# Kernel tuning notes

Measured on AMD Instinct MI355X. Metric: run time of the kernel, lower is better.

The kernel has to match this reference:

```python
import jax, jax.numpy as jnp
import numpy as np

NEG_SLOPE = 0.2  # PyG GATConv default leaky_relu slope
EPS = 1e-16


def gat_conv(x, W, att_src, att_dst, bias, src, dst, num_nodes, heads, out_ch, concat):
    # x: [N, F_in]; W: [F_in, heads*out_ch]
    h = (x @ W).reshape(num_nodes, heads, out_ch)          # [N, H, C]
    a_src = jnp.sum(h * att_src, axis=-1)                  # [N, H]
    a_dst = jnp.sum(h * att_dst, axis=-1)                  # [N, H]
    alpha = jax.nn.leaky_relu(a_src[src] + a_dst[dst], NEG_SLOPE)  # [E, H]
    # segment softmax over incoming edges of each destination node
    amax = jax.ops.segment_max(alpha, dst, num_segments=num_nodes)  # [N, H]
    ex = jnp.exp(alpha - amax[dst])                        # [E, H]
    denom = jax.ops.segment_sum(ex, dst, num_segments=num_nodes)    # [N, H]
    attn = ex / (denom[dst] + EPS)                         # [E, H]
    msg = h[src] * attn[:, :, None]                        # [E, H, C]
    out = jax.ops.segment_sum(msg, dst, num_segments=num_nodes)     # [N, H, C]
    if concat:
        out = out.reshape(num_nodes, heads * out_ch)
    else:
        out = out.mean(axis=1)
    return out + bias


def setup_inputs() -> dict:
    key = jax.random.key(0)
    ks = jax.random.split(key, 10)
    N, E, F_in, H, C, OUT = 50000, 800000, 512, 4, 64, 40
    x = jax.random.normal(ks[0], (N, F_in), dtype=jnp.float32)
    edge_index = jax.random.randint(ks[1], (2, E), 0, N, dtype=jnp.int64)
    s1 = (2.0 / (F_in + H * C)) ** 0.5
    s2 = (2.0 / (H * C + OUT)) ** 0.5
    return {
        "x": x,
        "edge_index": edge_index,
        "W1": jax.random.normal(ks[2], (F_in, H * C), dtype=jnp.float32) * s1,
        "att_src1": jax.random.normal(ks[3], (H, C), dtype=jnp.float32) * 0.1,
        "att_dst1": jax.random.normal(ks[4], (H, C), dtype=jnp.float32) * 0.1,
        "b1": jnp.zeros((H * C,), dtype=jnp.float32),
        "W2": jax.random.normal(ks[5], (H * C, OUT), dtype=jnp.float32) * s2,
        "att_src2": jax.random.normal(ks[6], (1, OUT), dtype=jnp.float32) * 0.1,
        "att_dst2": jax.random.normal(ks[7], (1, OUT), dtype=jnp.float32) * 0.1,
        "b2": jnp.zeros((OUT,), dtype=jnp.float32),
    }


def reference(x, edge_index, W1, att_src1, att_dst1, b1, W2, att_src2, att_dst2, b2):
    N = x.shape[0]
    H, C = att_src1.shape
    OUT = att_src2.shape[1]
    # PyG GATConv default: add self-loops
    loops = jnp.arange(N, dtype=edge_index.dtype)
    src = jnp.concatenate([edge_index[0], loops])
    dst = jnp.concatenate([edge_index[1], loops])
    # dropout is identity in eval mode
    h = gat_conv(x, W1, att_src1, att_dst1, b1, src, dst, N, H, C, concat=True)
    h = jax.nn.elu(h)
    out = gat_conv(h, W2, att_src2, att_dst2, b2, src, dst, N, 1, OUT, concat=False)
    return jax.nn.log_softmax(out, axis=1)
```

## Files before the change

kernel.cpp:

```cpp
#include <hip/hip_runtime.h>
#include <math.h>

#define FIN   512
#define H1DIM 256
#define HEADS 4
#define CH    64
#define OUTC  40
#define NEG   0.2f
#define EPSV  1e-16f
#define BK    64

__device__ __forceinline__ float leaky(float a) { return fmaxf(a, NEG * a); }

__device__ __forceinline__ short f2bf(float f) {
    unsigned u = __builtin_bit_cast(unsigned, f);
    u += 0x7FFFu + ((u >> 16) & 1u);
    return (short)(u >> 16);
}
__device__ __forceinline__ float bf2f(short s) {
    return __builtin_bit_cast(float, ((unsigned)(unsigned short)s) << 16);
}
__device__ __forceinline__ unsigned cvtpk(float lo, float hi) {
    unsigned r;
    asm("v_cvt_pk_bf16_f32 %0, %1, %2" : "=v"(r) : "v"(lo), "v"(hi));
    return r;
}
__device__ __forceinline__ float lo16(unsigned u) {
    return __builtin_bit_cast(float, u << 16);
}
__device__ __forceinline__ float hi16(unsigned u) {
    return __builtin_bit_cast(float, u & 0xffff0000u);
}

typedef __attribute__((ext_vector_type(2))) float floatx2;

__device__ __forceinline__ unsigned f32x2_to_fp8x2(float a, float b) {
    return (unsigned)__builtin_amdgcn_cvt_pk_fp8_f32(a, b, 0, false);
}
template <bool HI>
__device__ __forceinline__ floatx2 fp8x2_to_f32(unsigned u) {
    return __builtin_amdgcn_cvt_pk_f32_fp8((int)u, HI);
}

typedef __attribute__((ext_vector_type(8))) short short8;
typedef __attribute__((ext_vector_type(4))) short short4_t;
typedef __attribute__((ext_vector_type(4))) float float4_t;

typedef unsigned int u32;
typedef const __attribute__((address_space(1))) u32 gu32;
typedef __attribute__((address_space(3))) u32 lu32;

__device__ __forceinline__ void load_lds16(const void* g, void* l) {
    __builtin_amdgcn_global_load_lds((gu32*)g, (lu32*)l, 16, 0, 0);
}

__global__ void cvt_w1_kernel(const float* __restrict__ W1, short* __restrict__ w1t)
{
    int idx = blockIdx.x * 256 + threadIdx.x;
    if (idx >= FIN * H1DIM) return;
    int k = idx >> 8;
    int n = idx & 255;
    w1t[(size_t)n * FIN + k] = f2bf(W1[idx]);
}

__global__ __launch_bounds__(256, 1) void gemm1_mfma_kernel(
    const float* __restrict__ x, const short* __restrict__ w1t,
    const float* __restrict__ attS, const float* __restrict__ attD,
    unsigned char* __restrict__ h1f, float* __restrict__ aS1, float* __restrict__ aD1, int N)
{
    __shared__ float As[64 * 512];

    const int tid  = threadIdx.x;
    const int lane = tid & 63;
    const int wid  = tid >> 6;
    const int row0 = blockIdx.x * 64;
    const int col0 = wid * 64;
    const int quad = lane >> 4;
    const int m16  = lane & 15;

#pragma unroll
    for (int inst = 0; inst < 32; ++inst) {
        int c   = inst * 256 + tid;
        int row = c >> 7;
        int q   = (c & 127) ^ (row & 7);
        int gr  = row0 + row; if (gr >= N) gr = N - 1;
        load_lds16(x + (size_t)gr * FIN + q * 4, (char*)As + c * 16);
    }
    __syncthreads();

    const short* bp[4];
#pragma unroll
    for (int j = 0; j < 4; ++j)
        bp[j] = w1t + (size_t)(col0 + j * 16 + m16) * FIN + quad * 8;

    float4_t acc[4][4];
#pragma unroll
    for (int i = 0; i < 4; ++i)
#pragma unroll
        for (int j = 0; j < 4; ++j) acc[i][j] = (float4_t){0.f, 0.f, 0.f, 0.f};

    short8 bcur[2][4];
#pragma unroll
    for (int half = 0; half < 2; ++half)
#pragma unroll
        for (int j = 0; j < 4; ++j)
            bcur[half][j] = *(const short8*)(bp[j] + half * 32);

#pragma unroll
    for (int kk = 0; kk < FIN / BK; ++kk) {
        short8 bnext[2][4];
        if (kk < FIN / BK - 1) {
#pragma unroll
            for (int half = 0; half < 2; ++half)
#pragma unroll
                for (int j = 0; j < 4; ++j)
                    bnext[half][j] = *(const short8*)(bp[j] + (kk + 1) * BK + half * 32);
        }
#pragma unroll
        for (int half = 0; half < 2; ++half) {
            short8 a[4];
#pragma unroll
            for (int i = 0; i < 4; ++i) {
                int row = i * 16 + m16;
                int cb  = kk * 16 + (quad + 4 * half) * 2;
                const char* rp = (const char*)As + row * 2048;
                float4 f0 = *(const float4*)(rp + ((cb ^ (row & 7)) * 16));
                float4 f1 = *(const float4*)(rp + (((cb + 1) ^ (row & 7)) * 16));
                unsigned* tp = (unsigned*)&a[i];
                tp[0] = cvtpk(f0.x, f0.y);
                tp[1] = cvtpk(f0.z, f0.w);
                tp[2] = cvtpk(f1.x, f1.y);
                tp[3] = cvtpk(f1.z, f1.w);
            }
#pragma unroll
            for (int i = 0; i < 4; ++i)
#pragma unroll
                for (int j = 0; j < 4; ++j)
                    acc[i][j] = __builtin_amdgcn_mfma_f32_16x16x32_bf16(a[i], bcur[half][j], acc[i][j], 0, 0, 0);
        }
        if (kk < FIN / BK - 1) {
#pragma unroll
            for (int half = 0; half < 2; ++half)
#pragma unroll
                for (int j = 0; j < 4; ++j)
                    bcur[half][j] = bnext[half][j];
        }
    }

    float attSv[4], attDv[4];
#pragma unroll
    for (int j = 0; j < 4; ++j) {
        attSv[j] = attS[col0 + j * 16 + m16];
        attDv[j] = attD[col0 + j * 16 + m16];
    }

    __syncthreads();
    unsigned char* Asb = (unsigned char*)As;

#pragma unroll
    for (int i = 0; i < 4; ++i) {
#pragma unroll
        for (int r = 0; r < 4; ++r) {
            int rloc = i * 16 + quad * 4 + r;
            unsigned pa = f32x2_to_fp8x2(acc[i][0][r], acc[i][1][r]);
            unsigned pb = f32x2_to_fp8x2(acc[i][2][r], acc[i][3][r]);
            int cb = rloc * 256 + col0 + m16;
            Asb[cb]      = (unsigned char)(pa & 0xff);
            Asb[cb + 16] = (unsigned char)((pa >> 8) & 0xff);
            Asb[cb + 32] = (unsigned char)(pb & 0xff);
            Asb[cb + 48] = (unsigned char)((pb >> 8) & 0xff);

            float ps = acc[i][0][r] * attSv[0] + acc[i][1][r] * attSv[1]
                     + acc[i][2][r] * attSv[2] + acc[i][3][r] * attSv[3];
            float pd = acc[i][0][r] * attDv[0] + acc[i][1][r] * attDv[1]
                     + acc[i][2][r] * attDv[2] + acc[i][3][r] * attDv[3];
#pragma unroll
            for (int off = 1; off < 16; off <<= 1) {
                ps += __shfl_xor(ps, off);
                pd += __shfl_xor(pd, off);
            }
            int row = row0 + rloc;
            if (m16 == 0 && row < N) {
                aS1[(size_t)row * 4 + wid] = ps;
                aD1[(size_t)row * 4 + wid] = pd;
            }
        }
    }
    __syncthreads();

#pragma unroll
    for (int inst = 0; inst < 4; ++inst) {
        int flat = inst * 4096 + tid * 16;
        int row  = flat >> 8;
        if (row0 + row < N)
            *(float4*)(h1f + (size_t)row0 * H1DIM + flat) = *(const float4*)(Asb + flat);
    }
}

__global__ void degcount_kernel(const int* __restrict__ ei, int* __restrict__ deg,
                                int* __restrict__ rank, int E, int Etot)
{
    int e = blockIdx.x * 256 + threadIdx.x;
    if (e >= Etot) return;
    int d = (e < E) ? ei[E + e] : (e - E);
    rank[e] = atomicAdd(&deg[d], 1);
}

__global__ __launch_bounds__(1024) void scan_partial_kernel(
    const int* __restrict__ deg, int* __restrict__ offsets,
    int* __restrict__ bsums, int N)
{
    __shared__ int wsums[16];
    __shared__ int excl[16];
    int tid = threadIdx.x, lane = tid & 63, wid = tid >> 6;
    int idx = blockIdx.x * 1024 + tid;
    int v = (idx < N) ? deg[idx] : 0;
    int sv = v;
#pragma unroll
    for (int off = 1; off < 64; off <<= 1) {
        int t = __shfl_up(sv, off, 64);
        if (lane >= off) sv += t;
    }
    if (lane == 63) wsums[wid] = sv;
    __syncthreads();
    if (wid == 0 && lane < 16) {
        int wv = wsums[lane];
        int sw = wv;
#pragma unroll
        for (int off = 1; off < 16; off <<= 1) {
            int t = __shfl_up(sw, off, 64);
            if (lane >= off) sw += t;
        }
        excl[lane] = sw - wv;
        if (lane == 15) bsums[blockIdx.x] = sw;
    }
    __syncthreads();
    if (idx < N) offsets[idx + 1] = sv + excl[wid];
}

__global__ __launch_bounds__(1024) void scan_tops_kernel(
    int* __restrict__ bsums, int* __restrict__ boffs, int nb)
{
    __shared__ int wsums[16];
    __shared__ int excl[16];
    int tid = threadIdx.x, lane = tid & 63, wid = tid >> 6;
    int v = (tid < nb) ? bsums[tid] : 0;
    int sv = v;
#pragma unroll
    for (int off = 1; off < 64; off <<= 1) {
        int t = __shfl_up(sv, off, 64);
        if (lane >= off) sv += t;
    }
    if (lane == 63) wsums[wid] = sv;
    __syncthreads();
    if (wid == 0 && lane < 16) {
        int wv = wsums[lane];
        int sw = wv;
#pragma unroll
        for (int off = 1; off < 16; off <<= 1) {
            int t = __shfl_up(sw, off, 64);
            if (lane >= off) sw += t;
        }
        excl[lane] = sw - wv;
    }
    __syncthreads();
    if (tid < nb) boffs[tid] = sv + excl[wid] - v;
}

__global__ __launch_bounds__(1024) void scan_add_kernel(
    int* __restrict__ offsets, const int* __restrict__ boffs, int N)
{
    int idx = blockIdx.x * 1024 + threadIdx.x;
    if (idx == 0) offsets[0] = 0;
    if (idx < N) offsets[idx + 1] += boffs[blockIdx.x];
}

__global__ void scatter_kernel(const int* __restrict__ ei, const int* __restrict__ offsets,
                               const int* __restrict__ rank, int* __restrict__ csr_src,
                               int E, int Etot)
{
    int e = blockIdx.x * 256 + threadIdx.x;
    if (e >= Etot) return;
    int s, d;
    if (e < E) { s = ei[e]; d = ei[E + e]; }
    else       { s = e - E; d = s; }
    csr_src[offsets[d] + rank[e]] = s;
}

__global__ __launch_bounds__(256) void agg1_kernel(
    const unsigned char* __restrict__ h1f, const float* __restrict__ aS,
    const float* __restrict__ aD, const int* __restrict__ offsets,
    const int* __restrict__ csr_src, const float* __restrict__ b1,
    short* __restrict__ g1b, int N)
{
    int lane = threadIdx.x & 63, wid = threadIdx.x >> 6;
    int half = lane >> 5;
    int l32  = lane & 31;
    int n = blockIdx.x * 4 + wid;
    if (n >= N) return;
    int start = offsets[n], end = offsets[n + 1];
    int h = l32 >> 3;
    int cbase = l32 * 8;
    float adh = aD[(size_t)n * 4 + h];

    float ac[8];
#pragma unroll
    for (int c = 0; c < 8; ++c) ac[c] = 0.f;
    float denom = 0.f;

    int p = start;
    for (; p + 4 <= end; p += 4) {
        int sA0 = csr_src[p],     sB0 = csr_src[p + 1];
        int sA1 = csr_src[p + 2], sB1 = csr_src[p + 3];
        int s0 = half ? sB0 : sA0;
        int s1 = half ? sB1 : sA1;
        float t0 = aS[(size_t)s0 * 4 + h] + adh;
        float t1 = aS[(size_t)s1 * 4 + h] + adh;
        uint2 r0 = *(const uint2*)&h1f[(size_t)s0 * H1DIM + cbase];
        uint2 r1 = *(const uint2*)&h1f[(size_t)s1 * H1DIM + cbase];
        float w0 = __expf(leaky(t0));
        float w1 = __expf(leaky(t1));
        denom += w0 + w1;
        floatx2 d0a = fp8x2_to_f32<false>(r0.x), d0b = fp8x2_to_f32<true>(r0.x);
        floatx2 d0c = fp8x2_to_f32<false>(r0.y), d0d = fp8x2_to_f32<true>(r0.y);
        floatx2 d1a = fp8x2_to_f32<false>(r1.x), d1b = fp8x2_to_f32<true>(r1.x);
        floatx2 d1c = fp8x2_to_f32<false>(r1.y), d1d = fp8x2_to_f32<true>(r1.y);
        ac[0] += w0 * d0a.x + w1 * d1a.x;
        ac[1] += w0 * d0a.y + w1 * d1a.y;
        ac[2] += w0 * d0b.x + w1 * d1b.x;
        ac[3] += w0 * d0b.y + w1 * d1b.y;
        ac[4] += w0 * d0c.x + w1 * d1c.x;
        ac[5] += w0 * d0c.y + w1 * d1c.y;
        ac[6] += w0 * d0d.x + w1 * d1d.x;
        ac[7] += w0 * d0d.y + w1 * d1d.y;
    }
    for (; p + 2 <= end; p += 2) {
        int sA = csr_src[p], sB = csr_src[p + 1];
        int s = half ? sB : sA;
        float t = aS[(size_t)s * 4 + h] + adh;
        uint2 r = *(const uint2*)&h1f[(size_t)s * H1DIM + cbase];
        float w = __expf(leaky(t));
        denom += w;
        floatx2 da = fp8x2_to_f32<false>(r.x), db = fp8x2_to_f32<true>(r.x);
        floatx2 dc = fp8x2_to_f32<false>(r.y), dd = fp8x2_to_f32<true>(r.y);
        ac[0] += w * da.x; ac[1] += w * da.y;
        ac[2] += w * db.x; ac[3] += w * db.y;
        ac[4] += w * dc.x; ac[5] += w * dc.y;
        ac[6] += w * dd.x; ac[7] += w * dd.y;
    }
    if (p < end) {
        int s = csr_src[p];
        float t = aS[(size_t)s * 4 + h] + adh;
        uint2 r = *(const uint2*)&h1f[(size_t)s * H1DIM + cbase];
        float w = half ? 0.f : __expf(leaky(t));
        denom += w;
        floatx2 da = fp8x2_to_f32<false>(r.x), db = fp8x2_to_f32<true>(r.x);
        floatx2 dc = fp8x2_to_f32<false>(r.y), dd = fp8x2_to_f32<true>(r.y);
        ac[0] += w * da.x; ac[1] += w * da.y;
        ac[2] += w * db.x; ac[3] += w * db.y;
        ac[4] += w * dc.x; ac[5] += w * dc.y;
        ac[6] += w * dd.x; ac[7] += w * dd.y;
    }

    denom += __shfl_xor(denom, 32);
#pragma unroll
    for (int c = 0; c < 8; ++c) ac[c] += __shfl_xor(ac[c], 32);

    if (half == 0) {
        float inv = 1.f / (denom + EPSV);
        float4 b0 = *(const float4*)&b1[cbase];
        float4 b4 = *(const float4*)&b1[cbase + 4];
        float v[8];
        v[0] = ac[0] * inv + b0.x;
        v[1] = ac[1] * inv + b0.y;
        v[2] = ac[2] * inv + b0.z;
        v[3] = ac[3] * inv + b0.w;
        v[4] = ac[4] * inv + b4.x;
        v[5] = ac[5] * inv + b4.y;
        v[6] = ac[6] * inv + b4.z;
        v[7] = ac[7] * inv + b4.w;
#pragma unroll
        for (int c = 0; c < 8; ++c) v[c] = v[c] > 0.f ? v[c] : expm1f(v[c]);
        short8 o;
        unsigned* op = (unsigned*)&o;
        op[0] = cvtpk(v[0], v[1]);
        op[1] = cvtpk(v[2], v[3]);
        op[2] = cvtpk(v[4], v[5]);
        op[3] = cvtpk(v[6], v[7]);
        *(short8*)&g1b[(size_t)n * H1DIM + cbase] = o;
    }
}

__global__ __launch_bounds__(256) void gemm2_kernel(
    const short* __restrict__ g1b, const float* __restrict__ W2,
    const float* __restrict__ attS2, const float* __restrict__ attD2,
    short* __restrict__ h2b, float* __restrict__ aS2, float* __restrict__ aD2, int N)
{
    __shared__ float rows[4][8][256];
    int lane = threadIdx.x & 63, wid = threadIdx.x >> 6;
    int nbase = blockIdx.x * 32 + wid * 8;
    bool act = lane < OUTC;
    int cc = act ? lane : 0;
    float attS = act ? attS2[lane] : 0.f;
    float attD = act ? attD2[lane] : 0.f;

#pragma unroll
    for (int i = 0; i < 8; ++i) {
        int n = nbase + i;
        float4 v = make_float4(0.f, 0.f, 0.f, 0.f);
        if (n < N) {
            short4_t hv = *(const short4_t*)&g1b[(size_t)n * H1DIM + lane * 4];
            v = make_float4(bf2f(hv[0]), bf2f(hv[1]), bf2f(hv[2]), bf2f(hv[3]));
        }
        *(float4*)&rows[wid][i][lane * 4] = v;
    }

    float acc[8];
#pragma unroll
    for (int i = 0; i < 8; ++i) acc[i] = 0.f;

    for (int k = 0; k < H1DIM; k += 4) {
        float w0 = W2[(size_t)(k + 0) * OUTC + cc];
        float w1 = W2[(size_t)(k + 1) * OUTC + cc];
        float w2 = W2[(size_t)(k + 2) * OUTC + cc];
        float w3 = W2[(size_t)(k + 3) * OUTC + cc];
#pragma unroll
        for (int i = 0; i < 8; ++i) {
            float4 g = *(const float4*)&rows[wid][i][k];
            acc[i] += g.x * w0 + g.y * w1 + g.z * w2 + g.w * w3;
        }
    }

#pragma unroll
    for (int i = 0; i < 8; ++i) {
        int n = nbase + i;
        if (n >= N) continue;
        if (act) h2b[(size_t)n * OUTC + lane] = f2bf(acc[i]);
        float ts = act ? acc[i] * attS : 0.f;
        float td = act ? acc[i] * attD : 0.f;
#pragma unroll
        for (int off = 32; off > 0; off >>= 1) {
            ts += __shfl_xor(ts, off);
            td += __shfl_xor(td, off);
        }
        if (lane == 0) { aS2[n] = ts; aD2[n] = td; }
    }
}

__global__ __launch_bounds__(256) void agg2_kernel(
    const short* __restrict__ h2b, const float* __restrict__ aS2,
    const float* __restrict__ aD2, const int* __restrict__ offsets,
    const int* __restrict__ csr_src, const float* __restrict__ b2,
    float* __restrict__ out, int N)
{
    int lane = threadIdx.x & 63, wid = threadIdx.x >> 6;
    int n = blockIdx.x * 4 + wid;
    if (n >= N) return;
    int start = offsets[n], end = offsets[n + 1];
    bool act = lane < OUTC;
    int cc = act ? lane : 0;
    float ad = aD2[n];

    float acc = 0.f, denom = 0.f;
    int p = start;
    for (; p + 4 <= end; p += 4) {
        int s0 = csr_src[p], s1 = csr_src[p + 1], s2 = csr_src[p + 2], s3 = csr_src[p + 3];
        float w0 = __expf(leaky(aS2[s0] + ad));
        float w1 = __expf(leaky(aS2[s1] + ad));
        float w2 = __expf(leaky(aS2[s2] + ad));
        float w3 = __expf(leaky(aS2[s3] + ad));
        short v0 = h2b[(size_t)s0 * OUTC + cc];
        short v1 = h2b[(size_t)s1 * OUTC + cc];
        short v2 = h2b[(size_t)s2 * OUTC + cc];
        short v3 = h2b[(size_t)s3 * OUTC + cc];
        denom += w0 + w1 + w2 + w3;
        acc += w0 * bf2f(v0) + w1 * bf2f(v1) + w2 * bf2f(v2) + w3 * bf2f(v3);
    }
    for (; p < end; ++p) {
        int s = csr_src[p];
        float w = __expf(leaky(aS2[s] + ad));
        denom += w;
        acc += w * bf2f(h2b[(size_t)s * OUTC + cc]);
    }

    float v = acc / (denom + EPSV) + (act ? b2[lane] : 0.f);

    float vm = act ? v : -INFINITY;
#pragma unroll
    for (int off = 32; off > 0; off >>= 1) vm = fmaxf(vm, __shfl_xor(vm, off));
    float ex2 = act ? __expf(v - vm) : 0.f;
    float tot = ex2;
#pragma unroll
    for (int off = 32; off > 0; off >>= 1) tot += __shfl_xor(tot, off);
    float res = v - vm - __logf(tot);
    if (act) out[(size_t)n * OUTC + lane] = res;
}

extern "C" void kernel_launch(void* const* d_in, const int* in_sizes, int n_in,
                              void* d_out, int out_size, void* d_ws, size_t ws_size,
                              hipStream_t stream)
{
    const float* x     = (const float*)d_in[0];
    const int*   ei    = (const int*)d_in[1];
    const float* W1    = (const float*)d_in[2];
    const float* attS1 = (const float*)d_in[3];
    const float* attD1 = (const float*)d_in[4];
    const float* b1    = (const float*)d_in[5];
    const float* W2    = (const float*)d_in[6];
    const float* attS2 = (const float*)d_in[7];
    const float* attD2 = (const float*)d_in[8];
    const float* b2    = (const float*)d_in[9];
    float* out = (float*)d_out;

    const int N    = in_sizes[0] / FIN;
    const int E    = in_sizes[1] / 2;
    const int Etot = E + N;
    const int nb   = (N + 1023) / 1024;

    char* ws = (char*)d_ws;
    size_t off = 0;
    auto take = [&](size_t bytes) -> char* {
        char* p = ws + off;
        off = (off + bytes + 255) & ~(size_t)255;
        return p;
    };
    unsigned char* h1f = (unsigned char*)take((size_t)N * H1DIM);
    short* g1b     = (short*)take((size_t)N * H1DIM * 2);
    short* w1t     = (short*)take((size_t)FIN * H1DIM * 2);
    float* aS1     = (float*)take((size_t)N * 4 * 4);
    float* aD1     = (float*)take((size_t)N * 4 * 4);
    short* h2b     = (short*)take((size_t)N * OUTC * 2);
    float* aS2v    = (float*)take((size_t)N * 4);
    float* aD2v    = (float*)take((size_t)N * 4);
    int*   deg     = (int*)take((size_t)N * 4);
    int*   offsets = (int*)take((size_t)(N + 1) * 4);
    int*   bsums   = (int*)take((size_t)nb * 4);
    int*   boffs   = (int*)take((size_t)nb * 4);
    int*   rank    = (int*)take((size_t)Etot * 4);
    int*   csr_src = (int*)take((size_t)Etot * 4);

    (void)hipMemsetAsync(deg, 0, (size_t)N * 4, stream);

    cvt_w1_kernel<<<(FIN * H1DIM + 255) / 256, 256, 0, stream>>>(W1, w1t);
    gemm1_mfma_kernel<<<(N + 63) / 64, 256, 0, stream>>>(x, w1t, attS1, attD1, h1f, aS1, aD1, N);
    degcount_kernel<<<(Etot + 255) / 256, 256, 0, stream>>>(ei, deg, rank, E, Etot);
    scan_partial_kernel<<<nb, 1024, 0, stream>>>(deg, offsets, bsums, N);
    scan_tops_kernel<<<1, 1024, 0, stream>>>(bsums, boffs, nb);
    scan_add_kernel<<<nb, 1024, 0, stream>>>(offsets, boffs, N);
    scatter_kernel<<<(Etot + 255) / 256, 256, 0, stream>>>(ei, offsets, rank, csr_src, E, Etot);
    agg1_kernel<<<(N + 3) / 4, 256, 0, stream>>>(h1f, aS1, aD1, offsets, csr_src, b1, g1b, N);
    gemm2_kernel<<<(N + 31) / 32, 256, 0, stream>>>(g1b, W2, attS2, attD2, h2b, aS2v, aD2v, N);
    agg2_kernel<<<(N + 3) / 4, 256, 0, stream>>>(h2b, aS2v, aD2v, offsets, csr_src, b2, out, N);
}
```

Baseline: 427.1 us.

## Shrink GEMM1 tile to 32 rows and load x directly from global memory

```diff
diff --git a/kernel.cpp b/kernel.cpp
--- a/kernel.cpp
+++ b/kernel.cpp
@@ -25,12 +25,6 @@
     asm("v_cvt_pk_bf16_f32 %0, %1, %2" : "=v"(r) : "v"(lo), "v"(hi));
     return r;
 }
-__device__ __forceinline__ float lo16(unsigned u) {
-    return __builtin_bit_cast(float, u << 16);
-}
-__device__ __forceinline__ float hi16(unsigned u) {
-    return __builtin_bit_cast(float, u & 0xffff0000u);
-}
 
 typedef __attribute__((ext_vector_type(2))) float floatx2;
 
@@ -45,14 +39,6 @@
 typedef __attribute__((ext_vector_type(8))) short short8;
 typedef __attribute__((ext_vector_type(4))) short short4_t;
 typedef __attribute__((ext_vector_type(4))) float float4_t;
-
-typedef unsigned int u32;
-typedef const __attribute__((address_space(1))) u32 gu32;
-typedef __attribute__((address_space(3))) u32 lu32;
-
-__device__ __forceinline__ void load_lds16(const void* g, void* l) {
-    __builtin_amdgcn_global_load_lds((gu32*)g, (lu32*)l, 16, 0, 0);
-}
 
 __global__ void cvt_w1_kernel(const float* __restrict__ W1, short* __restrict__ w1t)
 {
@@ -63,69 +49,50 @@
     w1t[(size_t)n * FIN + k] = f2bf(W1[idx]);
 }
 
-__global__ __launch_bounds__(256, 1) void gemm1_mfma_kernel(
+__global__ __launch_bounds__(256, 4) void gemm1_mfma_kernel(
     const float* __restrict__ x, const short* __restrict__ w1t,
     const float* __restrict__ attS, const float* __restrict__ attD,
     unsigned char* __restrict__ h1f, float* __restrict__ aS1, float* __restrict__ aD1, int N)
 {
-    __shared__ float As[64 * 512];
+    __shared__ unsigned char Bounce[32 * 256];
 
     const int tid  = threadIdx.x;
     const int lane = tid & 63;
     const int wid  = tid >> 6;
-    const int row0 = blockIdx.x * 64;
+    const int row0 = blockIdx.x * 32;
     const int col0 = wid * 64;
     const int quad = lane >> 4;
     const int m16  = lane & 15;
 
-#pragma unroll
-    for (int inst = 0; inst < 32; ++inst) {
-        int c   = inst * 256 + tid;
-        int row = c >> 7;
-        int q   = (c & 127) ^ (row & 7);
-        int gr  = row0 + row; if (gr >= N) gr = N - 1;
-        load_lds16(x + (size_t)gr * FIN + q * 4, (char*)As + c * 16);
-    }
-    __syncthreads();
+    const float* ap[2];
+#pragma unroll
+    for (int i = 0; i < 2; ++i) {
+        int r = row0 + i * 16 + m16;
+        if (r >= N) r = N - 1;
+        ap[i] = x + (size_t)r * FIN + quad * 8;
+    }
 
     const short* bp[4];
 #pragma unroll
     for (int j = 0; j < 4; ++j)
         bp[j] = w1t + (size_t)(col0 + j * 16 + m16) * FIN + quad * 8;
 
-    float4_t acc[4][4];
-#pragma unroll
-    for (int i = 0; i < 4; ++i)
+    float4_t acc[2][4];
+#pragma unroll
+    for (int i = 0; i < 2; ++i)
 #pragma unroll
         for (int j = 0; j < 4; ++j) acc[i][j] = (float4_t){0.f, 0.f, 0.f, 0.f};
 
-    short8 bcur[2][4];
-#pragma unroll
-    for (int half = 0; half < 2; ++half)
-#pragma unroll
-        for (int j = 0; j < 4; ++j)
-            bcur[half][j] = *(const short8*)(bp[j] + half * 32);
-
 #pragma unroll
     for (int kk = 0; kk < FIN / BK; ++kk) {
-        short8 bnext[2][4];
-        if (kk < FIN / BK - 1) {
-#pragma unroll
-            for (int half = 0; half < 2; ++half)
-#pragma unroll
-                for (int j = 0; j < 4; ++j)
-                    bnext[half][j] = *(const short8*)(bp[j] + (kk + 1) * BK + half * 32);
-        }
 #pragma unroll
         for (int half = 0; half < 2; ++half) {
-            short8 a[4];
-#pragma unroll
-            for (int i = 0; i < 4; ++i) {
-                int row = i * 16 + m16;
-                int cb  = kk * 16 + (quad + 4 * half) * 2;
-                const char* rp = (const char*)As + row * 2048;
-                float4 f0 = *(const float4*)(rp + ((cb ^ (row & 7)) * 16));
-                float4 f1 = *(const float4*)(rp + (((cb + 1) ^ (row & 7)) * 16));
+            const int koff = kk * BK + half * 32;
+            short8 a[2], b[4];
+#pragma unroll
+            for (int i = 0; i < 2; ++i) {
+                float4 f0 = *(const float4*)(ap[i] + koff);
+                float4 f1 = *(const float4*)(ap[i] + koff + 4);
                 unsigned* tp = (unsigned*)&a[i];
                 tp[0] = cvtpk(f0.x, f0.y);
                 tp[1] = cvtpk(f0.z, f0.w);
@@ -133,17 +100,13 @@
                 tp[3] = cvtpk(f1.z, f1.w);
             }
 #pragma unroll
-            for (int i = 0; i < 4; ++i)
+            for (int j = 0; j < 4; ++j)
+                b[j] = *(const short8*)(bp[j] + koff);
+#pragma unroll
+            for (int i = 0; i < 2; ++i)
 #pragma unroll
                 for (int j = 0; j < 4; ++j)
-                    acc[i][j] = __builtin_amdgcn_mfma_f32_16x16x32_bf16(a[i], bcur[half][j], acc[i][j], 0, 0, 0);
-        }
-        if (kk < FIN / BK - 1) {
-#pragma unroll
-            for (int half = 0; half < 2; ++half)
-#pragma unroll
-                for (int j = 0; j < 4; ++j)
-                    bcur[half][j] = bnext[half][j];
+                    acc[i][j] = __builtin_amdgcn_mfma_f32_16x16x32_bf16(a[i], b[j], acc[i][j], 0, 0, 0);
         }
     }
 
@@ -154,21 +117,18 @@
         attDv[j] = attD[col0 + j * 16 + m16];
     }
 
-    __syncthreads();
-    unsigned char* Asb = (unsigned char*)As;
-
-#pragma unroll
-    for (int i = 0; i < 4; ++i) {
+#pragma unroll
+    for (int i = 0; i < 2; ++i) {
 #pragma unroll
         for (int r = 0; r < 4; ++r) {
             int rloc = i * 16 + quad * 4 + r;
             unsigned pa = f32x2_to_fp8x2(acc[i][0][r], acc[i][1][r]);
             unsigned pb = f32x2_to_fp8x2(acc[i][2][r], acc[i][3][r]);
             int cb = rloc * 256 + col0 + m16;
-            Asb[cb]      = (unsigned char)(pa & 0xff);
-            Asb[cb + 16] = (unsigned char)((pa >> 8) & 0xff);
-            Asb[cb + 32] = (unsigned char)(pb & 0xff);
-            Asb[cb + 48] = (unsigned char)((pb >> 8) & 0xff);
+            Bounce[cb]      = (unsigned char)(pa & 0xff);
+            Bounce[cb + 16] = (unsigned char)((pa >> 8) & 0xff);
+            Bounce[cb + 32] = (unsigned char)(pb & 0xff);
+            Bounce[cb + 48] = (unsigned char)((pb >> 8) & 0xff);
 
             float ps = acc[i][0][r] * attSv[0] + acc[i][1][r] * attSv[1]
                      + acc[i][2][r] * attSv[2] + acc[i][3][r] * attSv[3];
@@ -189,11 +149,11 @@
     __syncthreads();
 
 #pragma unroll
-    for (int inst = 0; inst < 4; ++inst) {
+    for (int inst = 0; inst < 2; ++inst) {
         int flat = inst * 4096 + tid * 16;
         int row  = flat >> 8;
         if (row0 + row < N)
-            *(float4*)(h1f + (size_t)row0 * H1DIM + flat) = *(const float4*)(Asb + flat);
+            *(float4*)(h1f + (size_t)row0 * H1DIM + flat) = *(const float4*)(Bounce + flat);
     }
 }
 
@@ -542,7 +502,7 @@
     (void)hipMemsetAsync(deg, 0, (size_t)N * 4, stream);
 
     cvt_w1_kernel<<<(FIN * H1DIM + 255) / 256, 256, 0, stream>>>(W1, w1t);
-    gemm1_mfma_kernel<<<(N + 63) / 64, 256, 0, stream>>>(x, w1t, attS1, attD1, h1f, aS1, aD1, N);
+    gemm1_mfma_kernel<<<(N + 31) / 32, 256, 0, stream>>>(x, w1t, attS1, attD1, h1f, aS1, aD1, N);
     degcount_kernel<<<(Etot + 255) / 256, 256, 0, stream>>>(ei, deg, rank, E, Etot);
     scan_partial_kernel<<<nb, 1024, 0, stream>>>(deg, offsets, bsums, N);
     scan_tops_kernel<<<1, 1024, 0, stream>>>(bsums, boffs, nb);
```

Measured after the change: 464.5 us. +8.8%, slower.
